# Kernel optimization log

Measured on AMD Instinct MI355X. Metric: run time of the kernel, lower is better.

The kernel has to match this reference:

```python
import jax, jax.numpy as jnp
import numpy as np

B, L, D, V = 64, 512, 768, 100
LN_EPS = 1e-6


def setup_inputs() -> dict:
    key = jax.random.key(0)
    k1, k2, k3, k4 = jax.random.split(key, 4)
    return {
        "ids": jax.random.randint(k1, (B, 1), 0, V),
        "pooler": jax.random.normal(k2, (B, L, D), dtype=jnp.float32),
        "emb_table": jax.random.normal(k3, (V, 2), dtype=jnp.float32),
        "W_dense": jax.random.normal(k4, (2, D), dtype=jnp.float32) * 0.1,
        "b_dense": jnp.zeros((D,), dtype=jnp.float32),
        "gamma": jnp.ones((D,), dtype=jnp.float32),
        "beta": jnp.zeros((D,), dtype=jnp.float32),
    }


def reference(ids, pooler, emb_table, W_dense, b_dense, gamma, beta):
    # id -> 2-dim projection -> dense to embed_dim: xt (B, 1, D)
    emb = emb_table[ids]                      # (B, 1, 2)
    xt = emb @ W_dense + b_dense              # (B, 1, D)

    # Per timestep i the original concatenates [pooler[:, i], xt] into a
    # 2-token sequence and runs dot-product self-attention (keras Attention,
    # no scaling), then sums over the 2 tokens. Vectorized over all L steps:
    tok = jnp.stack([pooler, jnp.broadcast_to(xt, pooler.shape)], axis=2)  # (B, L, 2, D)
    scores = jnp.einsum('blqd,blkd->blqk', tok, tok)                       # (B, L, 2, 2)
    attn = jax.nn.softmax(scores, axis=-1)
    out = jnp.einsum('blqk,blkd->blqd', attn, tok)                         # (B, L, 2, D)
    summed = out.sum(axis=2)                                               # (B, L, D)

    # dropout is identity at inference; layernorm over last axis, eps=1e-6
    mean = summed.mean(axis=-1, keepdims=True)
    var = summed.var(axis=-1, keepdims=True)
    normed = (summed - mean) * jax.lax.rsqrt(var + LN_EPS)
    return normed * gamma + beta
```

## Files before the change

### kernel.cpp

```cpp
#include <hip/hip_runtime.h>


constexpr int Bc = 64;
constexpr int Lc = 512;
constexpr int Dc = 768;
constexpr float LN_EPS = 1e-6f;
constexpr int WAVES_PER_BLOCK = 4;
constexpr int ROWS_PER_WAVE   = 4;
constexpr int ROWS_PER_BLOCK  = WAVES_PER_BLOCK * ROWS_PER_WAVE;

typedef float nv_float4 __attribute__((ext_vector_type(4)));

__global__ __launch_bounds__(64 * WAVES_PER_BLOCK, 4) void hier_attn_ln_kernel(
    const int*   __restrict__ ids,
    const float* __restrict__ pooler,
    const float* __restrict__ emb_table,
    const float* __restrict__ W,
    const float* __restrict__ bvec,
    const float* __restrict__ gamma,
    const float* __restrict__ beta,
    float*       __restrict__ out)
{
    const int wave = threadIdx.x >> 6;
    const int lane = threadIdx.x & 63;
    const int row0 = blockIdx.x * ROWS_PER_BLOCK + wave * ROWS_PER_WAVE;
    const int b    = row0 >> 9;

    const float4* W0_4 = (const float4*)W;
    const float4* W1_4 = (const float4*)(W + Dc);
    const float4* b_4  = (const float4*)bvec;
    const float4* g_4  = (const float4*)gamma;
    const float4* be_4 = (const float4*)beta;

    const int id = ids[b];
    const float e0 = emb_table[id * 2 + 0];
    const float e1 = emb_table[id * 2 + 1];

    const float4* p_base = (const float4*)(pooler + (size_t)row0 * Dc);
    nv_float4*    o_base = (nv_float4*)(out + (size_t)row0 * Dc);

    float4 t[ROWS_PER_WAVE][3];
#pragma unroll
    for (int r = 0; r < ROWS_PER_WAVE; ++r)
#pragma unroll
        for (int j = 0; j < 3; ++j)
            t[r][j] = p_base[r * (Dc / 4) + lane + j * 64];

    float4 xt[3];
    float s11 = 0.f, S1 = 0.f;
#pragma unroll
    for (int j = 0; j < 3; ++j) {
        const int idx4 = lane + j * 64;
        float4 w0 = W0_4[idx4];
        float4 w1 = W1_4[idx4];
        float4 bd = b_4[idx4];
        float4 x;
        x.x = fmaf(e0, w0.x, fmaf(e1, w1.x, bd.x));
        x.y = fmaf(e0, w0.y, fmaf(e1, w1.y, bd.y));
        x.z = fmaf(e0, w0.z, fmaf(e1, w1.z, bd.z));
        x.w = fmaf(e0, w0.w, fmaf(e1, w1.w, bd.w));
        xt[j] = x;
        s11 += x.x*x.x + x.y*x.y + x.z*x.z + x.w*x.w;
        S1  += x.x + x.y + x.z + x.w;
    }

    float s00[ROWS_PER_WAVE], s01[ROWS_PER_WAVE], S0[ROWS_PER_WAVE];
#pragma unroll
    for (int r = 0; r < ROWS_PER_WAVE; ++r) {
        float a0 = 0.f, a1 = 0.f, a2 = 0.f;
#pragma unroll
        for (int j = 0; j < 3; ++j) {
            const float4 p = t[r][j];
            a0 += p.x*p.x + p.y*p.y + p.z*p.z + p.w*p.w;
            a1 += p.x*xt[j].x + p.y*xt[j].y + p.z*xt[j].z + p.w*xt[j].w;
            a2 += p.x + p.y + p.z + p.w;
        }
        s00[r] = a0; s01[r] = a1; S0[r] = a2;
    }

#pragma unroll
    for (int off = 32; off > 0; off >>= 1) {
        s11 += __shfl_xor(s11, off);
        S1  += __shfl_xor(S1,  off);
#pragma unroll
        for (int r = 0; r < ROWS_PER_WAVE; ++r) {
            s00[r] += __shfl_xor(s00[r], off);
            s01[r] += __shfl_xor(s01[r], off);
            S0[r]  += __shfl_xor(S0[r],  off);
        }
    }

    float4 gm[3], bt[3];
#pragma unroll
    for (int j = 0; j < 3; ++j) {
        gm[j] = g_4[lane + j * 64];
        bt[j] = be_4[lane + j * 64];
    }

    const float invD = 1.f / (float)Dc;
    float ascale[ROWS_PER_WAVE], cscale[ROWS_PER_WAVE], mshift[ROWS_PER_WAVE];
#pragma unroll
    for (int r = 0; r < ROWS_PER_WAVE; ++r) {
        const float m0  = fmaxf(s00[r], s01[r]);
        const float a00 = __expf(s00[r] - m0);
        const float a01 = __expf(s01[r] - m0);
        const float r0  = 1.f / (a00 + a01);
        const float m1  = fmaxf(s01[r], s11);
        const float a10 = __expf(s01[r] - m1);
        const float a11 = __expf(s11 - m1);
        const float r1  = 1.f / (a10 + a11);
        const float w0s = a00 * r0 + a10 * r1;
        const float w1s = a01 * r0 + a11 * r1;

        const float mean = (w0s * S0[r] + w1s * S1) * invD;
        const float ex2  = (w0s*w0s*s00[r] + 2.f*w0s*w1s*s01[r] + w1s*w1s*s11) * invD;
        const float var  = ex2 - mean * mean;
        const float rstd = rsqrtf(var + LN_EPS);

        ascale[r] = w0s * rstd;
        cscale[r] = w1s * rstd;
        mshift[r] = mean * rstd;
    }

#pragma unroll
    for (int r = 0; r < ROWS_PER_WAVE; ++r) {
        const float a = ascale[r], c = cscale[r], m = mshift[r];
        nv_float4* orow4 = o_base + (size_t)r * (Dc / 4);
#pragma unroll
        for (int j = 0; j < 3; ++j) {
            nv_float4 o;
            o.x = fmaf(gm[j].x, fmaf(a, t[r][j].x, fmaf(c, xt[j].x, -m)), bt[j].x);
            o.y = fmaf(gm[j].y, fmaf(a, t[r][j].y, fmaf(c, xt[j].y, -m)), bt[j].y);
            o.z = fmaf(gm[j].z, fmaf(a, t[r][j].z, fmaf(c, xt[j].z, -m)), bt[j].z);
            o.w = fmaf(gm[j].w, fmaf(a, t[r][j].w, fmaf(c, xt[j].w, -m)), bt[j].w);
            __builtin_nontemporal_store(o, &orow4[lane + j * 64]);
        }
    }
}

extern "C" void kernel_launch(void* const* d_in, const int* in_sizes, int n_in,
                              void* d_out, int out_size, void* d_ws, size_t ws_size,
                              hipStream_t stream) {
    const int*   ids       = (const int*)  d_in[0];
    const float* pooler    = (const float*)d_in[1];
    const float* emb_table = (const float*)d_in[2];
    const float* W_dense   = (const float*)d_in[3];
    const float* b_dense   = (const float*)d_in[4];
    const float* gamma     = (const float*)d_in[5];
    const float* beta      = (const float*)d_in[6];
    float* out = (float*)d_out;

    const int nrows = Bc * Lc;
    hipLaunchKernelGGL(hier_attn_ln_kernel,
                       dim3(nrows / ROWS_PER_BLOCK), dim3(64 * WAVES_PER_BLOCK),
                       0, stream,
                       ids, pooler, emb_table, W_dense, b_dense, gamma, beta, out);
}
```

Before: 193.3 us.

## Split fused attention-layernorm into scalar-stats pass and apply pass

Result: slower. 202.4 us (+4.7%).

```diff
diff --git a/kernel.cpp b/kernel.cpp
--- a/kernel.cpp
+++ b/kernel.cpp
@@ -5,55 +5,39 @@
 constexpr int Lc = 512;
 constexpr int Dc = 768;
 constexpr float LN_EPS = 1e-6f;
-constexpr int WAVES_PER_BLOCK = 4;
-constexpr int ROWS_PER_WAVE   = 4;
-constexpr int ROWS_PER_BLOCK  = WAVES_PER_BLOCK * ROWS_PER_WAVE;
+constexpr int WPB = 4;
+constexpr int RPW = 4;
+constexpr int RPB = WPB * RPW;
 
 typedef float nv_float4 __attribute__((ext_vector_type(4)));
 
-__global__ __launch_bounds__(64 * WAVES_PER_BLOCK, 4) void hier_attn_ln_kernel(
+__global__ __launch_bounds__(64 * WPB) void pass1_scalars(
     const int*   __restrict__ ids,
     const float* __restrict__ pooler,
     const float* __restrict__ emb_table,
     const float* __restrict__ W,
     const float* __restrict__ bvec,
-    const float* __restrict__ gamma,
-    const float* __restrict__ beta,
-    float*       __restrict__ out)
+    float4*      __restrict__ ws)
 {
     const int wave = threadIdx.x >> 6;
     const int lane = threadIdx.x & 63;
-    const int row0 = blockIdx.x * ROWS_PER_BLOCK + wave * ROWS_PER_WAVE;
+    const int row0 = blockIdx.x * RPB + wave * RPW;
     const int b    = row0 >> 9;
 
     const float4* W0_4 = (const float4*)W;
     const float4* W1_4 = (const float4*)(W + Dc);
     const float4* b_4  = (const float4*)bvec;
-    const float4* g_4  = (const float4*)gamma;
-    const float4* be_4 = (const float4*)beta;
 
     const int id = ids[b];
     const float e0 = emb_table[id * 2 + 0];
     const float e1 = emb_table[id * 2 + 1];
 
-    const float4* p_base = (const float4*)(pooler + (size_t)row0 * Dc);
-    nv_float4*    o_base = (nv_float4*)(out + (size_t)row0 * Dc);
-
-    float4 t[ROWS_PER_WAVE][3];
-#pragma unroll
-    for (int r = 0; r < ROWS_PER_WAVE; ++r)
-#pragma unroll
-        for (int j = 0; j < 3; ++j)
-            t[r][j] = p_base[r * (Dc / 4) + lane + j * 64];
-
     float4 xt[3];
     float s11 = 0.f, S1 = 0.f;
 #pragma unroll
     for (int j = 0; j < 3; ++j) {
-        const int idx4 = lane + j * 64;
-        float4 w0 = W0_4[idx4];
-        float4 w1 = W1_4[idx4];
-        float4 bd = b_4[idx4];
+        const int i4 = lane + j * 64;
+        float4 w0 = W0_4[i4], w1 = W1_4[i4], bd = b_4[i4];
         float4 x;
         x.x = fmaf(e0, w0.x, fmaf(e1, w1.x, bd.x));
         x.y = fmaf(e0, w0.y, fmaf(e1, w1.y, bd.y));
@@ -64,13 +48,14 @@
         S1  += x.x + x.y + x.z + x.w;
     }
 
-    float s00[ROWS_PER_WAVE], s01[ROWS_PER_WAVE], S0[ROWS_PER_WAVE];
-#pragma unroll
-    for (int r = 0; r < ROWS_PER_WAVE; ++r) {
+    const float4* p_base = (const float4*)(pooler + (size_t)row0 * Dc);
+    float s00[RPW], s01[RPW], S0[RPW];
+#pragma unroll
+    for (int r = 0; r < RPW; ++r) {
         float a0 = 0.f, a1 = 0.f, a2 = 0.f;
 #pragma unroll
         for (int j = 0; j < 3; ++j) {
-            const float4 p = t[r][j];
+            const float4 p = p_base[r * (Dc / 4) + lane + j * 64];
             a0 += p.x*p.x + p.y*p.y + p.z*p.z + p.w*p.w;
             a1 += p.x*xt[j].x + p.y*xt[j].y + p.z*xt[j].z + p.w*xt[j].w;
             a2 += p.x + p.y + p.z + p.w;
@@ -83,57 +68,113 @@
         s11 += __shfl_xor(s11, off);
         S1  += __shfl_xor(S1,  off);
 #pragma unroll
-        for (int r = 0; r < ROWS_PER_WAVE; ++r) {
+        for (int r = 0; r < RPW; ++r) {
             s00[r] += __shfl_xor(s00[r], off);
             s01[r] += __shfl_xor(s01[r], off);
             S0[r]  += __shfl_xor(S0[r],  off);
         }
     }
 
-    float4 gm[3], bt[3];
+    const int r = lane & 3;
+    const float t00 = (r & 1) ? s00[1] : s00[0];
+    const float u00 = (r & 1) ? s00[3] : s00[2];
+    const float v00 = (r & 2) ? u00 : t00;
+    const float t01 = (r & 1) ? s01[1] : s01[0];
+    const float u01 = (r & 1) ? s01[3] : s01[2];
+    const float v01 = (r & 2) ? u01 : t01;
+    const float tS0 = (r & 1) ? S0[1] : S0[0];
+    const float uS0 = (r & 1) ? S0[3] : S0[2];
+    const float vS0 = (r & 2) ? uS0 : tS0;
+
+    const float m0  = fmaxf(v00, v01);
+    const float a00 = __expf(v00 - m0);
+    const float a01 = __expf(v01 - m0);
+    const float r0  = 1.f / (a00 + a01);
+    const float m1  = fmaxf(v01, s11);
+    const float a10 = __expf(v01 - m1);
+    const float a11 = __expf(s11 - m1);
+    const float r1  = 1.f / (a10 + a11);
+    const float w0s = a00 * r0 + a10 * r1;
+    const float w1s = a01 * r0 + a11 * r1;
+
+    const float invD = 1.f / (float)Dc;
+    const float mean = (w0s * vS0 + w1s * S1) * invD;
+    const float ex2  = (w0s*w0s*v00 + 2.f*w0s*w1s*v01 + w1s*w1s*s11) * invD;
+    const float var  = ex2 - mean * mean;
+    const float rstd = rsqrtf(var + LN_EPS);
+
+    if (lane < 4) {
+        float4 o;
+        o.x = w0s * rstd;
+        o.y = w1s * rstd;
+        o.z = mean * rstd;
+        o.w = 0.f;
+        ws[row0 + r] = o;
+    }
+}
+
+__global__ __launch_bounds__(64 * WPB) void pass2_apply(
+    const int*   __restrict__ ids,
+    const float* __restrict__ pooler,
+    const float* __restrict__ emb_table,
+    const float* __restrict__ W,
+    const float* __restrict__ bvec,
+    const float* __restrict__ gamma,
+    const float* __restrict__ beta,
+    const float4* __restrict__ ws,
+    float*       __restrict__ out)
+{
+    const int wave = threadIdx.x >> 6;
+    const int lane = threadIdx.x & 63;
+    const int row0 = blockIdx.x * RPB + wave * RPW;
+    const int b    = row0 >> 9;
+
+    const float4* W0_4 = (const float4*)W;
+    const float4* W1_4 = (const float4*)(W + Dc);
+    const float4* b_4  = (const float4*)bvec;
+    const float4* g_4  = (const float4*)gamma;
+    const float4* be_4 = (const float4*)beta;
+
+    const int id = ids[b];
+    const float e0 = emb_table[id * 2 + 0];
+    const float e1 = emb_table[id * 2 + 1];
+
+    float4 xt[3], gm[3], bt[3];
 #pragma unroll
     for (int j = 0; j < 3; ++j) {
-        gm[j] = g_4[lane + j * 64];
-        bt[j] = be_4[lane + j * 64];
-    }
-
-    const float invD = 1.f / (float)Dc;
-    float ascale[ROWS_PER_WAVE], cscale[ROWS_PER_WAVE], mshift[ROWS_PER_WAVE];
-#pragma unroll
-    for (int r = 0; r < ROWS_PER_WAVE; ++r) {
-        const float m0  = fmaxf(s00[r], s01[r]);
-        const float a00 = __expf(s00[r] - m0);
-        const float a01 = __expf(s01[r] - m0);
-        const float r0  = 1.f / (a00 + a01);
-        const float m1  = fmaxf(s01[r], s11);
-        const float a10 = __expf(s01[r] - m1);
-        const float a11 = __expf(s11 - m1);
-        const float r1  = 1.f / (a10 + a11);
-        const float w0s = a00 * r0 + a10 * r1;
-        const float w1s = a01 * r0 + a11 * r1;
-
-        const float mean = (w0s * S0[r] + w1s * S1) * invD;
-        const float ex2  = (w0s*w0s*s00[r] + 2.f*w0s*w1s*s01[r] + w1s*w1s*s11) * invD;
-        const float var  = ex2 - mean * mean;
-        const float rstd = rsqrtf(var + LN_EPS);
-
-        ascale[r] = w0s * rstd;
-        cscale[r] = w1s * rstd;
-        mshift[r] = mean * rstd;
-    }
-
-#pragma unroll
-    for (int r = 0; r < ROWS_PER_WAVE; ++r) {
-        const float a = ascale[r], c = cscale[r], m = mshift[r];
-        nv_float4* orow4 = o_base + (size_t)r * (Dc / 4);
+        const int i4 = lane + j * 64;
+        float4 w0 = W0_4[i4], w1 = W1_4[i4], bd = b_4[i4];
+        gm[j] = g_4[i4];
+        bt[j] = be_4[i4];
+        float4 x;
+        x.x = fmaf(e0, w0.x, fmaf(e1, w1.x, bd.x));
+        x.y = fmaf(e0, w0.y, fmaf(e1, w1.y, bd.y));
+        x.z = fmaf(e0, w0.z, fmaf(e1, w1.z, bd.z));
+        x.w = fmaf(e0, w0.w, fmaf(e1, w1.w, bd.w));
+        xt[j] = x;
+    }
+
+    float4 s[RPW];
+#pragma unroll
+    for (int r = 0; r < RPW; ++r) s[r] = ws[row0 + r];
+
+    const float4* p_base = (const float4*)(pooler + (size_t)row0 * Dc);
+    nv_float4*    o_base = (nv_float4*)(out + (size_t)row0 * Dc);
+
+#pragma unroll
+    for (int rr = 0; rr < RPW; ++rr) {
+        const float a = s[rr].x, c = s[rr].y, m = s[rr].z;
+        const float4* prow = p_base + (size_t)rr * (Dc / 4);
+        nv_float4*    orow = o_base + (size_t)rr * (Dc / 4);
 #pragma unroll
         for (int j = 0; j < 3; ++j) {
+            const float4 p = prow[lane + j * 64];
             nv_float4 o;
-            o.x = fmaf(gm[j].x, fmaf(a, t[r][j].x, fmaf(c, xt[j].x, -m)), bt[j].x);
-            o.y = fmaf(gm[j].y, fmaf(a, t[r][j].y, fmaf(c, xt[j].y, -m)), bt[j].y);
-            o.z = fmaf(gm[j].z, fmaf(a, t[r][j].z, fmaf(c, xt[j].z, -m)), bt[j].z);
-            o.w = fmaf(gm[j].w, fmaf(a, t[r][j].w, fmaf(c, xt[j].w, -m)), bt[j].w);
-            __builtin_nontemporal_store(o, &orow4[lane + j * 64]);
+            o.x = fmaf(gm[j].x, fmaf(a, p.x, fmaf(c, xt[j].x, -m)), bt[j].x);
+            o.y = fmaf(gm[j].y, fmaf(a, p.y, fmaf(c, xt[j].y, -m)), bt[j].y);
+            o.z = fmaf(gm[j].z, fmaf(a, p.z, fmaf(c, xt[j].z, -m)), bt[j].z);
+            o.w = fmaf(gm[j].w, fmaf(a, p.w, fmaf(c, xt[j].w, -m)), bt[j].w);
+            __builtin_nontemporal_store(o, &orow[lane + j * 64]);
         }
     }
 }
@@ -149,10 +190,14 @@
     const float* gamma     = (const float*)d_in[5];
     const float* beta      = (const float*)d_in[6];
     float* out = (float*)d_out;
-
-    const int nrows = Bc * Lc;
-    hipLaunchKernelGGL(hier_attn_ln_kernel,
-                       dim3(nrows / ROWS_PER_BLOCK), dim3(64 * WAVES_PER_BLOCK),
-                       0, stream,
-                       ids, pooler, emb_table, W_dense, b_dense, gamma, beta, out);
+    float4* ws = (float4*)d_ws;
+
+    const int nrows  = Bc * Lc;
+    const int nblk   = nrows / RPB;
+
+    hipLaunchKernelGGL(pass1_scalars, dim3(nblk), dim3(64 * WPB), 0, stream,
+                       ids, pooler, emb_table, W_dense, b_dense, ws);
+    hipLaunchKernelGGL(pass2_apply, dim3(nblk), dim3(64 * WPB), 0, stream,
+                       ids, pooler, emb_table, W_dense, b_dense, gamma, beta,
+                       ws, out);
 }
```
